# Kernel tuning notes

Measured on AMD Instinct MI355X. Metric: run time of the kernel, lower is better.

The kernel has to match this reference:

```python
import jax, jax.numpy as jnp
import numpy as np

N = 100000      # nodes
E = 1600000     # edges
F = 64          # num_features
C = 10          # num_classes
L = 4           # num_layers
B = 128         # graphs in batch


def setup_inputs() -> dict:
    key = jax.random.key(0)
    ks = jax.random.split(key, 8)
    x = jax.random.normal(ks[0], (N, F), dtype=jnp.float32)
    edge_index = jax.random.randint(ks[1], (2, E), 0, N, dtype=jnp.int64)
    batch = jnp.sort(jax.random.randint(ks[2], (N,), 0, B, dtype=jnp.int64))
    scale = 1.0 / jnp.sqrt(jnp.float32(F))
    W1s = jax.random.normal(ks[3], (L, F, F), dtype=jnp.float32) * scale
    W2s = jax.random.normal(ks[4], (L, F, F), dtype=jnp.float32) * scale
    fc_w = jax.random.normal(ks[5], (C, F), dtype=jnp.float32) * scale
    fc_b = jax.random.normal(ks[6], (C,), dtype=jnp.float32) * 0.01
    return {"x": x, "edge_index": edge_index, "batch": batch,
            "W1s": W1s, "W2s": W2s, "fc_w": fc_w, "fc_b": fc_b}


def reference(x, edge_index, batch, W1s, W2s, fc_w, fc_b):
    src, dst = edge_index[0], edge_index[1]
    h = x
    for l in range(L):  # small fixed layer count
        # GINConv, eps=0: (1+eps)*x + sum of neighbor features (gather + scatter-add)
        agg = jax.ops.segment_sum(h[src], dst, num_segments=N)
        h = agg + h
        # MLP([F,F,F], bias=False, plain_last=False, act=sigmoid): two linears, each followed by sigmoid
        h = jax.nn.sigmoid(h @ W1s[l])
        h = jax.nn.sigmoid(h @ W2s[l])
    # global_add_pool over graphs in the batch
    xr = jax.ops.segment_sum(h, batch, num_segments=B)  # [B, F]
    logits = xr @ fc_w.T + fc_b                          # [B, C]
    return jax.nn.log_softmax(logits, axis=1), xr
```

## Files before the change

### kernel.cpp

```cpp
#include <hip/hip_runtime.h>
#include <hip/hip_bf16.h>

#define NN 100000
#define NE 1600000
#define FF 64
#define NC 10
#define NL 4
#define NB 128
#define LDST 72
#define CAP 48
#define NW 196
#define WCAPE 8704
#define PB_BIN 196
#define PB_XF 782
#define PB_W 32
#define PB_TOTAL (PB_BIN + PB_XF + PB_W + 1)

typedef __attribute__((ext_vector_type(8))) short short8;
typedef __attribute__((ext_vector_type(8))) unsigned short ushort8;
typedef __attribute__((ext_vector_type(4))) float f32x4;
typedef __attribute__((ext_vector_type(2))) float f32x2;
typedef __attribute__((ext_vector_type(4))) int int4v;

static __device__ __forceinline__ unsigned short f2bf(float x) {
  unsigned int u = __float_as_uint(x);
  unsigned int r = (u + 0x7fffu + ((u >> 16) & 1u)) >> 16;
  return (unsigned short)r;
}
static __device__ __forceinline__ float bf2f(unsigned short u) {
  return __uint_as_float(((unsigned int)u) << 16);
}
static __device__ __forceinline__ uint2 pack_f8(const float* a) {
  int w0 = __builtin_amdgcn_cvt_pk_fp8_f32(a[0], a[1], 0, false);
  w0 = __builtin_amdgcn_cvt_pk_fp8_f32(a[2], a[3], w0, true);
  int w1 = __builtin_amdgcn_cvt_pk_fp8_f32(a[4], a[5], 0, false);
  w1 = __builtin_amdgcn_cvt_pk_fp8_f32(a[6], a[7], w1, true);
  return make_uint2((unsigned)w0, (unsigned)w1);
}
static __device__ __forceinline__ void acc8w(f32x2* a, unsigned int x,
                                             unsigned int y) {
#if __has_builtin(__builtin_amdgcn_cvt_pk_f32_fp8)
  a[0] += __builtin_amdgcn_cvt_pk_f32_fp8((int)x, false);
  a[1] += __builtin_amdgcn_cvt_pk_f32_fp8((int)x, true);
  a[2] += __builtin_amdgcn_cvt_pk_f32_fp8((int)y, false);
  a[3] += __builtin_amdgcn_cvt_pk_f32_fp8((int)y, true);
#else
  a[0][0] += __builtin_amdgcn_cvt_f32_fp8((int)x, 0);
  a[0][1] += __builtin_amdgcn_cvt_f32_fp8((int)x, 1);
  a[1][0] += __builtin_amdgcn_cvt_f32_fp8((int)x, 2);
  a[1][1] += __builtin_amdgcn_cvt_f32_fp8((int)x, 3);
  a[2][0] += __builtin_amdgcn_cvt_f32_fp8((int)y, 0);
  a[2][1] += __builtin_amdgcn_cvt_f32_fp8((int)y, 1);
  a[3][0] += __builtin_amdgcn_cvt_f32_fp8((int)y, 2);
  a[3][1] += __builtin_amdgcn_cvt_f32_fp8((int)y, 3);
#endif
}
static __device__ __forceinline__ void acc16(f32x2* a, uint4 v) {
  acc8w(a, v.x, v.y);
  acc8w(a + 4, v.z, v.w);
}
static __device__ __forceinline__ unsigned char f2f8(float v) {
  return (unsigned char)(__builtin_amdgcn_cvt_pk_fp8_f32(v, v, 0, false) & 0xff);
}

__global__ __launch_bounds__(1024) void prepbin_kernel(
    const float* __restrict__ x, const int* __restrict__ src,
    const int* __restrict__ dst, const float* __restrict__ W1s,
    const float* __restrict__ W2s, uint2* __restrict__ xf8,
    unsigned short* __restrict__ Wt, int* __restrict__ wcnt,
    unsigned int* __restrict__ ebuf, uint2* __restrict__ hf8a,
    uint2* __restrict__ hf8b) {
  __shared__ int lcnt[NW];
  __shared__ int lbase[NW];
  int b = blockIdx.x;
  int t = threadIdx.x;
  if (b < PB_BIN) {
    int base = b * 8192 + t * 8;
    int d[8], s[8], wj[8];
    bool v[8];
    if (base + 8 <= NE) {
      *(int4*)(&d[0]) = *(const int4*)(dst + base);
      *(int4*)(&d[4]) = *(const int4*)(dst + base + 4);
      *(int4*)(&s[0]) = *(const int4*)(src + base);
      *(int4*)(&s[4]) = *(const int4*)(src + base + 4);
      #pragma unroll
      for (int j = 0; j < 8; ++j) v[j] = true;
    } else {
      #pragma unroll
      for (int j = 0; j < 8; ++j) {
        int e = base + j;
        v[j] = (e < NE);
        d[j] = v[j] ? dst[e] : 0;
        s[j] = v[j] ? src[e] : 0;
      }
    }
    #pragma unroll
    for (int j = 0; j < 8; ++j) wj[j] = d[j] >> 9;
    if (t < NW) lcnt[t] = 0;
    __syncthreads();
    #pragma unroll
    for (int j = 0; j < 8; ++j)
      if (v[j]) atomicAdd(&lcnt[wj[j]], 1);
    __syncthreads();
    if (t < NW) {
      lbase[t] = atomicAdd(&wcnt[t], lcnt[t]);
      lcnt[t] = 0;
    }
    __syncthreads();
    #pragma unroll
    for (int j = 0; j < 8; ++j) {
      if (v[j]) {
        int pos = lbase[wj[j]] + atomicAdd(&lcnt[wj[j]], 1);
        if (pos < WCAPE)
          ebuf[(size_t)wj[j] * WCAPE + pos] =
              ((unsigned)(d[j] & 511) << 17) | (unsigned)s[j];
      }
    }
  } else if (b < PB_BIN + PB_XF) {
    int g = (b - PB_BIN) * 1024 + t;
    if (g < NN * FF / 8) {
      size_t base = (size_t)g * 8;
      float4 a = *(const float4*)(x + base);
      float4 c = *(const float4*)(x + base + 4);
      float f[8] = {a.x, a.y, a.z, a.w, c.x, c.y, c.z, c.w};
      xf8[g] = pack_f8(f);
    }
  } else if (b < PB_BIN + PB_XF + PB_W) {
    int g = (b - PB_BIN - PB_XF) * 1024 + t;
    int mat = g >> 12, idx = g & 4095;
    int k = idx >> 6, n = idx & 63;
    int l = mat >> 1;
    const float* W = (mat & 1) ? (W2s + (size_t)l * FF * FF) : (W1s + (size_t)l * FF * FF);
    Wt[(size_t)mat * FF * FF + n * FF + k] = f2bf(W[k * FF + n]);
  } else {
    if (t < 8) {
      xf8[(size_t)NN * 8 + t] = make_uint2(0, 0);
      hf8a[(size_t)NN * 8 + t] = make_uint2(0, 0);
      hf8b[(size_t)NN * 8 + t] = make_uint2(0, 0);
    }
  }
}

__global__ __launch_bounds__(1024) void fillC_kernel(const unsigned int* __restrict__ ebuf,
                                                     const int* __restrict__ wcnt,
                                                     int* __restrict__ csr,
                                                     int* __restrict__ deg) {
  __shared__ int cur[512];
  int b = blockIdx.x;
  int t = threadIdx.x;
  int n0 = b << 9;
  if (t < 512) cur[t] = 0;
  __syncthreads();
  int cnt = min(wcnt[b], WCAPE);
  const unsigned int* ep = ebuf + (size_t)b * WCAPE;
  for (int i = t; i < cnt; i += 1024) {
    unsigned int e = ep[i];
    int dl = e >> 17;
    int s = (int)(e & 0x1ffffu);
    int slot = atomicAdd(&cur[dl], 1);
    if (slot < CAP) csr[(n0 + dl) * CAP + slot] = s;
  }
  __syncthreads();
  if (t < 512) {
    int node = n0 + t;
    if (node < NN) {
      int c = min(cur[t], CAP);
      deg[node] = c;
      int end = (c + 3) & ~3;
      for (; c < end; ++c) csr[node * CAP + c] = NN;
    }
  }
}

__global__ __launch_bounds__(256) void layer_kernel(
    const uint2* __restrict__ hin8, const int* __restrict__ csr,
    const int* __restrict__ deg, const unsigned short* __restrict__ Wt,
    uint2* __restrict__ hout8, const int* __restrict__ batch,
    float* __restrict__ xr, int last) {
  __shared__ __align__(16) unsigned short uL[64 * LDST];
  __shared__ __align__(16) unsigned char fb[64 * 64];
  int t = threadIdx.x;
  int row0 = blockIdx.x * 64;
  int lane = t & 63, w = t >> 6;
  int j2 = lane & 3;
  int gnode = lane >> 2;

  {
    int r = w * 16 + gnode;
    int node = row0 + r;
    f32x2 a[8] = {{0.f,0.f},{0.f,0.f},{0.f,0.f},{0.f,0.f},
                  {0.f,0.f},{0.f,0.f},{0.f,0.f},{0.f,0.f}};
    const uint4* hp4 = (const uint4*)hin8 + j2;
    if (node < NN) {
      acc16(a, hp4[(size_t)node * 4]);
      int i = node * CAP;
      int dg = deg[node];
      int endp = i + ((dg + 3) & ~3);
      int4v nxt = *(const int4v*)(csr + i);
      while (i < endp) {
        int4v cur = nxt;
        nxt = *(const int4v*)(csr + i + 4);
        uint4 r0 = hp4[(size_t)cur[0] * 4];
        uint4 r1 = hp4[(size_t)cur[1] * 4];
        uint4 r2 = hp4[(size_t)cur[2] * 4];
        uint4 r3 = hp4[(size_t)cur[3] * 4];
        acc16(a, r0); acc16(a, r1); acc16(a, r2); acc16(a, r3);
        i += 4;
      }
    }
    ushort8 u0, u1;
    #pragma unroll
    for (int kk = 0; kk < 8; ++kk) u0[kk] = f2bf(a[kk >> 1][kk & 1]);
    #pragma unroll
    for (int kk = 0; kk < 8; ++kk) u1[kk] = f2bf(a[4 + (kk >> 1)][kk & 1]);
    *(ushort8*)(&uL[r * LDST + j2 * 16]) = u0;
    *(ushort8*)(&uL[r * LDST + j2 * 16 + 8]) = u1;
  }

  __builtin_amdgcn_sched_barrier(0);

  int m = lane & 15, q = lane >> 4;
  short8 b1[4][2], b2[4][2];
  #pragma unroll
  for (int c4 = 0; c4 < 4; ++c4) {
    #pragma unroll
    for (int s = 0; s < 2; ++s) {
      b1[c4][s] = *(const short8*)(Wt + (c4 * 16 + m) * FF + s * 32 + q * 8);
      b2[c4][s] = *(const short8*)(Wt + FF * FF + (c4 * 16 + m) * FF + s * 32 + q * 8);
    }
  }

  f32x4 acc[4] = {{0,0,0,0},{0,0,0,0},{0,0,0,0},{0,0,0,0}};
  #pragma unroll
  for (int s = 0; s < 2; ++s) {
    short8 a = *(const short8*)(&uL[(w * 16 + m) * LDST + s * 32 + q * 8]);
    #pragma unroll
    for (int c4 = 0; c4 < 4; ++c4)
      acc[c4] = __builtin_amdgcn_mfma_f32_16x16x32_bf16(a, b1[c4][s], acc[c4], 0, 0, 0);
  }
  #pragma unroll
  for (int c4 = 0; c4 < 4; ++c4) {
    #pragma unroll
    for (int i = 0; i < 4; ++i) {
      int r = w * 16 + q * 4 + i;
      float sgv = 1.f / (1.f + __expf(-acc[c4][i]));
      uL[r * LDST + c4 * 16 + m] = f2bf(sgv);
    }
  }

  f32x4 acc2[4] = {{0,0,0,0},{0,0,0,0},{0,0,0,0},{0,0,0,0}};
  #pragma unroll
  for (int s = 0; s < 2; ++s) {
    short8 a = *(const short8*)(&uL[(w * 16 + m) * LDST + s * 32 + q * 8]);
    #pragma unroll
    for (int c4 = 0; c4 < 4; ++c4)
      acc2[c4] = __builtin_amdgcn_mfma_f32_16x16x32_bf16(a, b2[c4][s], acc2[c4], 0, 0, 0);
  }
  if (last) {
    #pragma unroll
    for (int c4 = 0; c4 < 4; ++c4) {
      #pragma unroll
      for (int i = 0; i < 4; ++i) {
        int r = w * 16 + q * 4 + i;
        float sgv = 1.f / (1.f + __expf(-acc2[c4][i]));
        uL[r * LDST + c4 * 16 + m] = f2bf(sgv);
      }
    }
    int r0 = w * 16;
    int node0 = row0 + r0;
    if (node0 < NN) {
      float pacc = 0.f;
      int cur = batch[node0];
      #pragma unroll
      for (int r = 0; r < 16; ++r) {
        int node = node0 + r;
        if (node < NN) {
          int bb = batch[node];
          if (bb != cur) {
            unsafeAtomicAdd(&xr[(size_t)cur * FF + lane], pacc);
            pacc = 0.f; cur = bb;
          }
          pacc += bf2f(uL[(r0 + r) * LDST + lane]);
        }
      }
      unsafeAtomicAdd(&xr[(size_t)cur * FF + lane], pacc);
    }
  } else {
    #pragma unroll
    for (int c4 = 0; c4 < 4; ++c4) {
      #pragma unroll
      for (int i = 0; i < 4; ++i) {
        int r = w * 16 + q * 4 + i;
        float sgv = 1.f / (1.f + __expf(-acc2[c4][i]));
        fb[r * 64 + c4 * 16 + m] = f2f8(sgv);
      }
    }
    {
      int r = w * 16 + gnode;
      int node = row0 + r;
      if (node < NN) {
        uint4 v = *(const uint4*)(fb + r * 64 + j2 * 16);
        uint4* hout4 = (uint4*)hout8;
        hout4[(size_t)node * 4 + j2] = v;
      }
    }
  }
}

__global__ __launch_bounds__(64) void head_kernel(
    const float* __restrict__ xr, const float* __restrict__ fcw,
    const float* __restrict__ fcb, float* __restrict__ out) {
  int b = blockIdx.x, lane = threadIdx.x;
  float v = xr[(size_t)b * FF + lane];
  out[NB * NC + (size_t)b * FF + lane] = v;
  float logit[NC];
  #pragma unroll
  for (int c = 0; c < NC; ++c) {
    float s = v * fcw[c * FF + lane];
    #pragma unroll
    for (int o = 32; o > 0; o >>= 1) s += __shfl_xor(s, o, 64);
    logit[c] = s + fcb[c];
  }
  float mx = logit[0];
  #pragma unroll
  for (int c = 1; c < NC; ++c) mx = fmaxf(mx, logit[c]);
  float se = 0.f;
  #pragma unroll
  for (int c = 0; c < NC; ++c) se += expf(logit[c] - mx);
  float lse = logf(se);
  if (lane < NC) out[b * NC + lane] = logit[lane] - mx - lse;
}

extern "C" void kernel_launch(void* const* d_in, const int* in_sizes, int n_in,
                              void* d_out, int out_size, void* d_ws, size_t ws_size,
                              hipStream_t stream) {
  const float* x     = (const float*)d_in[0];
  const int*   ei    = (const int*)d_in[1];
  const int*   batch = (const int*)d_in[2];
  const float* W1s   = (const float*)d_in[3];
  const float* W2s   = (const float*)d_in[4];
  const float* fcw   = (const float*)d_in[5];
  const float* fcb   = (const float*)d_in[6];
  float* out = (float*)d_out;

  char* p = (char*)d_ws;
  uint2* xf8  = (uint2*)p; p += (size_t)(NN + 1) * 8 * 8;
  uint2* hf8a = (uint2*)p; p += (size_t)(NN + 1) * 8 * 8;
  uint2* hf8b = (uint2*)p; p += (size_t)(NN + 1) * 8 * 8;
  int* csr    = (int*)p;   p += (size_t)NN * CAP * 4;
  unsigned int* ebuf = (unsigned int*)p; p += (size_t)NW * WCAPE * 4;
  int* deg    = (int*)p;   p += (size_t)NN * 4;
  int* wcnt   = (int*)p;   p += (size_t)((NW + 63) & ~63) * 4;
  float* xr   = (float*)p; p += (size_t)NB * FF * 4;
  unsigned short* Wtall = (unsigned short*)p; p += (size_t)2 * NL * FF * FF * 2;

  const int* src = ei;
  const int* dst = ei + NE;

  hipMemsetAsync(wcnt, 0,
                 (size_t)((NW + 63) & ~63) * 4 + (size_t)NB * FF * 4, stream);

  prepbin_kernel<<<PB_TOTAL, 1024, 0, stream>>>(
      x, src, dst, W1s, W2s, xf8, Wtall, wcnt, ebuf, hf8a, hf8b);

  fillC_kernel<<<NW, 1024, 0, stream>>>(ebuf, wcnt, csr, deg);

  int layer_blocks = (NN + 63) / 64;
  const uint2* chain_in[NL]  = {xf8, hf8a, hf8b, hf8a};
  uint2*       chain_out[NL] = {hf8a, hf8b, hf8a, hf8b};
  for (int l = 0; l < NL; ++l) {
    int last = (l == NL - 1) ? 1 : 0;
    layer_kernel<<<layer_blocks, 256, 0, stream>>>(chain_in[l], csr, deg,
        Wtall + (size_t)l * 2 * FF * FF, chain_out[l], batch, xr, last);
  }

  head_kernel<<<NB, 64, 0, stream>>>(xr, fcw, fcb, out);
}
```

Baseline: 266.6 us.

## Quantize inter-layer hidden features to 4-bit and aggregate with packed integer adds

```diff
diff --git a/kernel.cpp b/kernel.cpp
--- a/kernel.cpp
+++ b/kernel.cpp
@@ -59,17 +59,14 @@
   acc8w(a, v.x, v.y);
   acc8w(a + 4, v.z, v.w);
 }
-static __device__ __forceinline__ unsigned char f2f8(float v) {
-  return (unsigned char)(__builtin_amdgcn_cvt_pk_fp8_f32(v, v, 0, false) & 0xff);
-}
 
 __global__ __launch_bounds__(1024) void prepbin_kernel(
     const float* __restrict__ x, const int* __restrict__ src,
     const int* __restrict__ dst, const float* __restrict__ W1s,
     const float* __restrict__ W2s, uint2* __restrict__ xf8,
     unsigned short* __restrict__ Wt, int* __restrict__ wcnt,
-    unsigned int* __restrict__ ebuf, uint2* __restrict__ hf8a,
-    uint2* __restrict__ hf8b) {
+    unsigned int* __restrict__ ebuf, unsigned char* __restrict__ hq0,
+    unsigned char* __restrict__ hq1) {
   __shared__ int lcnt[NW];
   __shared__ int lbase[NW];
   int b = blockIdx.x;
@@ -135,8 +132,10 @@
   } else {
     if (t < 8) {
       xf8[(size_t)NN * 8 + t] = make_uint2(0, 0);
-      hf8a[(size_t)NN * 8 + t] = make_uint2(0, 0);
-      hf8b[(size_t)NN * 8 + t] = make_uint2(0, 0);
+    } else if (t < 12) {
+      ((uint2*)hq0)[(size_t)NN * 4 + (t - 8)] = make_uint2(0, 0);
+    } else if (t < 16) {
+      ((uint2*)hq1)[(size_t)NN * 4 + (t - 12)] = make_uint2(0, 0);
     }
   }
 }
@@ -172,10 +171,11 @@
   }
 }
 
+template <int IN4>
 __global__ __launch_bounds__(256) void layer_kernel(
-    const uint2* __restrict__ hin8, const int* __restrict__ csr,
+    const void* __restrict__ hin, const int* __restrict__ csr,
     const int* __restrict__ deg, const unsigned short* __restrict__ Wt,
-    uint2* __restrict__ hout8, const int* __restrict__ batch,
+    unsigned char* __restrict__ hout4, const int* __restrict__ batch,
     float* __restrict__ xr, int last) {
   __shared__ __align__(16) unsigned short uL[64 * LDST];
   __shared__ __align__(16) unsigned char fb[64 * 64];
@@ -188,31 +188,84 @@
   {
     int r = w * 16 + gnode;
     int node = row0 + r;
-    f32x2 a[8] = {{0.f,0.f},{0.f,0.f},{0.f,0.f},{0.f,0.f},
-                  {0.f,0.f},{0.f,0.f},{0.f,0.f},{0.f,0.f}};
-    const uint4* hp4 = (const uint4*)hin8 + j2;
-    if (node < NN) {
-      acc16(a, hp4[(size_t)node * 4]);
-      int i = node * CAP;
-      int dg = deg[node];
-      int endp = i + ((dg + 3) & ~3);
-      int4v nxt = *(const int4v*)(csr + i);
-      while (i < endp) {
-        int4v cur = nxt;
-        nxt = *(const int4v*)(csr + i + 4);
-        uint4 r0 = hp4[(size_t)cur[0] * 4];
-        uint4 r1 = hp4[(size_t)cur[1] * 4];
-        uint4 r2 = hp4[(size_t)cur[2] * 4];
-        uint4 r3 = hp4[(size_t)cur[3] * 4];
-        acc16(a, r0); acc16(a, r1); acc16(a, r2); acc16(a, r3);
-        i += 4;
-      }
-    }
     ushort8 u0, u1;
-    #pragma unroll
-    for (int kk = 0; kk < 8; ++kk) u0[kk] = f2bf(a[kk >> 1][kk & 1]);
-    #pragma unroll
-    for (int kk = 0; kk < 8; ++kk) u1[kk] = f2bf(a[4 + (kk >> 1)][kk & 1]);
+    if (IN4) {
+      float af[16];
+      #pragma unroll
+      for (int k = 0; k < 16; ++k) af[k] = 0.f;
+      if (node < NN) {
+        const uint2* hb = (const uint2*)hin;
+        uint2 sv = hb[(size_t)node * 4 + j2];
+        unsigned se0 = sv.x & 0x0F0F0F0Fu, so0 = (sv.x >> 4) & 0x0F0F0F0Fu;
+        unsigned se1 = sv.y & 0x0F0F0F0Fu, so1 = (sv.y >> 4) & 0x0F0F0F0Fu;
+        #pragma unroll
+        for (int k = 0; k < 4; ++k) {
+          af[2 * k]         = (float)((se0 >> (8 * k)) & 0xFFu);
+          af[2 * k + 1]     = (float)((so0 >> (8 * k)) & 0xFFu);
+          af[8 + 2 * k]     = (float)((se1 >> (8 * k)) & 0xFFu);
+          af[8 + 2 * k + 1] = (float)((so1 >> (8 * k)) & 0xFFu);
+        }
+        int i = node * CAP;
+        int dg = deg[node];
+        int endp = i + ((dg + 3) & ~3);
+        while (i < endp) {
+          unsigned pe0 = 0, po0 = 0, pe1 = 0, po1 = 0;
+          int stop = min(endp, i + 16);
+          for (; i < stop; i += 4) {
+            int4v x0 = *(const int4v*)(csr + i);
+            uint2 r0 = hb[(size_t)x0[0] * 4 + j2];
+            uint2 r1 = hb[(size_t)x0[1] * 4 + j2];
+            uint2 r2 = hb[(size_t)x0[2] * 4 + j2];
+            uint2 r3 = hb[(size_t)x0[3] * 4 + j2];
+            pe0 += r0.x & 0x0F0F0F0Fu; po0 += (r0.x >> 4) & 0x0F0F0F0Fu;
+            pe1 += r0.y & 0x0F0F0F0Fu; po1 += (r0.y >> 4) & 0x0F0F0F0Fu;
+            pe0 += r1.x & 0x0F0F0F0Fu; po0 += (r1.x >> 4) & 0x0F0F0F0Fu;
+            pe1 += r1.y & 0x0F0F0F0Fu; po1 += (r1.y >> 4) & 0x0F0F0F0Fu;
+            pe0 += r2.x & 0x0F0F0F0Fu; po0 += (r2.x >> 4) & 0x0F0F0F0Fu;
+            pe1 += r2.y & 0x0F0F0F0Fu; po1 += (r2.y >> 4) & 0x0F0F0F0Fu;
+            pe0 += r3.x & 0x0F0F0F0Fu; po0 += (r3.x >> 4) & 0x0F0F0F0Fu;
+            pe1 += r3.y & 0x0F0F0F0Fu; po1 += (r3.y >> 4) & 0x0F0F0F0Fu;
+          }
+          #pragma unroll
+          for (int k = 0; k < 4; ++k) {
+            af[2 * k]         += (float)((pe0 >> (8 * k)) & 0xFFu);
+            af[2 * k + 1]     += (float)((po0 >> (8 * k)) & 0xFFu);
+            af[8 + 2 * k]     += (float)((pe1 >> (8 * k)) & 0xFFu);
+            af[8 + 2 * k + 1] += (float)((po1 >> (8 * k)) & 0xFFu);
+          }
+        }
+      }
+      const float S = 1.f / 15.f;
+      #pragma unroll
+      for (int kk = 0; kk < 8; ++kk) u0[kk] = f2bf(af[kk] * S);
+      #pragma unroll
+      for (int kk = 0; kk < 8; ++kk) u1[kk] = f2bf(af[8 + kk] * S);
+    } else {
+      f32x2 a[8] = {{0.f,0.f},{0.f,0.f},{0.f,0.f},{0.f,0.f},
+                    {0.f,0.f},{0.f,0.f},{0.f,0.f},{0.f,0.f}};
+      const uint4* hp4 = (const uint4*)hin + j2;
+      if (node < NN) {
+        acc16(a, hp4[(size_t)node * 4]);
+        int i = node * CAP;
+        int dg = deg[node];
+        int endp = i + ((dg + 3) & ~3);
+        int4v nxt = *(const int4v*)(csr + i);
+        while (i < endp) {
+          int4v cur = nxt;
+          nxt = *(const int4v*)(csr + i + 4);
+          uint4 r0 = hp4[(size_t)cur[0] * 4];
+          uint4 r1 = hp4[(size_t)cur[1] * 4];
+          uint4 r2 = hp4[(size_t)cur[2] * 4];
+          uint4 r3 = hp4[(size_t)cur[3] * 4];
+          acc16(a, r0); acc16(a, r1); acc16(a, r2); acc16(a, r3);
+          i += 4;
+        }
+      }
+      #pragma unroll
+      for (int kk = 0; kk < 8; ++kk) u0[kk] = f2bf(a[kk >> 1][kk & 1]);
+      #pragma unroll
+      for (int kk = 0; kk < 8; ++kk) u1[kk] = f2bf(a[4 + (kk >> 1)][kk & 1]);
+    }
     *(ushort8*)(&uL[r * LDST + j2 * 16]) = u0;
     *(ushort8*)(&uL[r * LDST + j2 * 16 + 8]) = u1;
   }
@@ -292,16 +345,22 @@
       for (int i = 0; i < 4; ++i) {
         int r = w * 16 + q * 4 + i;
         float sgv = 1.f / (1.f + __expf(-acc2[c4][i]));
-        fb[r * 64 + c4 * 16 + m] = f2f8(sgv);
+        fb[r * 64 + c4 * 16 + m] = (unsigned char)(int)(sgv * 15.f + 0.5f);
       }
     }
     {
       int r = w * 16 + gnode;
       int node = row0 + r;
       if (node < NN) {
-        uint4 v = *(const uint4*)(fb + r * 64 + j2 * 16);
-        uint4* hout4 = (uint4*)hout8;
-        hout4[(size_t)node * 4 + j2] = v;
+        const unsigned* fp = (const unsigned*)(fb + r * 64 + j2 * 16);
+        unsigned x0 = fp[0], x1 = fp[1], x2 = fp[2], x3 = fp[3];
+        unsigned t0 = x0 | (x0 >> 4), t1 = x1 | (x1 >> 4);
+        unsigned t2 = x2 | (x2 >> 4), t3 = x3 | (x3 >> 4);
+        unsigned lo = (t0 & 0xFFu) | ((t0 >> 8) & 0xFF00u) |
+                      (((t1 & 0xFFu) | ((t1 >> 8) & 0xFF00u)) << 16);
+        unsigned hi = (t2 & 0xFFu) | ((t2 >> 8) & 0xFF00u) |
+                      (((t3 & 0xFFu) | ((t3 >> 8) & 0xFF00u)) << 16);
+        *(uint2*)(hout4 + (size_t)node * 32 + j2 * 8) = make_uint2(lo, hi);
       }
     }
   }
@@ -344,9 +403,9 @@
   float* out = (float*)d_out;
 
   char* p = (char*)d_ws;
-  uint2* xf8  = (uint2*)p; p += (size_t)(NN + 1) * 8 * 8;
-  uint2* hf8a = (uint2*)p; p += (size_t)(NN + 1) * 8 * 8;
-  uint2* hf8b = (uint2*)p; p += (size_t)(NN + 1) * 8 * 8;
+  uint2* xf8 = (uint2*)p;          p += (size_t)(NN + 1) * 64;
+  unsigned char* hq0 = (unsigned char*)p; p += (size_t)(NN + 1) * 32;
+  unsigned char* hq1 = (unsigned char*)p; p += (size_t)(NN + 1) * 32;
   int* csr    = (int*)p;   p += (size_t)NN * CAP * 4;
   unsigned int* ebuf = (unsigned int*)p; p += (size_t)NW * WCAPE * 4;
   int* deg    = (int*)p;   p += (size_t)NN * 4;
@@ -361,18 +420,19 @@
                  (size_t)((NW + 63) & ~63) * 4 + (size_t)NB * FF * 4, stream);
 
   prepbin_kernel<<<PB_TOTAL, 1024, 0, stream>>>(
-      x, src, dst, W1s, W2s, xf8, Wtall, wcnt, ebuf, hf8a, hf8b);
+      x, src, dst, W1s, W2s, xf8, Wtall, wcnt, ebuf, hq0, hq1);
 
   fillC_kernel<<<NW, 1024, 0, stream>>>(ebuf, wcnt, csr, deg);
 
   int layer_blocks = (NN + 63) / 64;
-  const uint2* chain_in[NL]  = {xf8, hf8a, hf8b, hf8a};
-  uint2*       chain_out[NL] = {hf8a, hf8b, hf8a, hf8b};
-  for (int l = 0; l < NL; ++l) {
-    int last = (l == NL - 1) ? 1 : 0;
-    layer_kernel<<<layer_blocks, 256, 0, stream>>>(chain_in[l], csr, deg,
-        Wtall + (size_t)l * 2 * FF * FF, chain_out[l], batch, xr, last);
-  }
+  layer_kernel<0><<<layer_blocks, 256, 0, stream>>>(
+      (const void*)xf8, csr, deg, Wtall + 0 * 2 * FF * FF, hq0, batch, xr, 0);
+  layer_kernel<1><<<layer_blocks, 256, 0, stream>>>(
+      (const void*)hq0, csr, deg, Wtall + 1 * 2 * FF * FF, hq1, batch, xr, 0);
+  layer_kernel<1><<<layer_blocks, 256, 0, stream>>>(
+      (const void*)hq1, csr, deg, Wtall + 2 * 2 * FF * FF, hq0, batch, xr, 0);
+  layer_kernel<1><<<layer_blocks, 256, 0, stream>>>(
+      (const void*)hq0, csr, deg, Wtall + 3 * 2 * FF * FF, hq1, batch, xr, 1);
 
   head_kernel<<<NB, 64, 0, stream>>>(xr, fcw, fcb, out);
 }
```

Result: faster. 245.9 us (-7.8%).
